# Kernel tuning notes

Measured on AMD Instinct MI355X. Metric: run time of the kernel, lower is better.

## Reference

```python
import jax, jax.numpy as jnp
import numpy as np

N, E, B, T, H, L = 8192, 2048, 512, 128, 128, 3


def setup_inputs() -> dict:
    key = jax.random.key(0)
    ks = jax.random.split(key, 14)
    # sparse binary hyperedge incidence [E, N]
    Hbat = (jax.random.uniform(ks[0], (E, N)) < 0.01).astype(jnp.float32)
    DV2 = jax.random.uniform(ks[1], (N,)) + 0.1    # D_v^{-1/2} node scaling
    invDE = jax.random.uniform(ks[2], (E,)) + 0.1  # D_e^{-1} edge scaling
    data = jax.random.randint(ks[3], (B, T), 0, N, dtype=jnp.int32)
    lens = jax.random.randint(ks[4], (B,), 1, T + 1, dtype=jnp.int32)
    data_length = jnp.sort(lens)[::-1].at[0].set(T)  # descending, max == T (pack_padded)
    poi = jax.random.normal(ks[5], (N, H), dtype=jnp.float32)
    s = 1.0 / float(np.sqrt(H))
    hgc1_w = jax.random.uniform(ks[6], (H, H), minval=-s, maxval=s)
    hgc1_b = jax.random.uniform(ks[7], (H,), minval=-s, maxval=s)
    hgc2_w = jax.random.uniform(ks[8], (H, H), minval=-s, maxval=s)
    hgc2_b = jax.random.uniform(ks[9], (H,), minval=-s, maxval=s)
    Wih = jax.random.uniform(ks[10], (L, 3 * H, H), minval=-s, maxval=s)
    Whh = jax.random.uniform(ks[11], (L, 3 * H, H), minval=-s, maxval=s)
    bih = jax.random.uniform(ks[12], (L, 3 * H), minval=-s, maxval=s)
    bhh = jax.random.uniform(ks[13], (L, 3 * H), minval=-s, maxval=s)
    return dict(Hbat=Hbat, DV2=DV2, invDE=invDE, data=data, data_length=data_length,
                poi=poi, hgc1_w=hgc1_w, hgc1_b=hgc1_b, hgc2_w=hgc2_w, hgc2_b=hgc2_b,
                Wih=Wih, Whh=Whh, bih=bih, bhh=bhh)


def _gru(x, Wih, Whh, bih, bhh):
    # torch nn.GRU (batch_first, 1 layer, h0=0). x: [B,T,H] -> [B,T,H]
    gx = jnp.einsum('bth,gh->btg', x, Wih) + bih  # precompute input gates [B,T,3H]

    def step(h, gxt):
        gh = h @ Whh.T + bhh
        xr, xz, xn = jnp.split(gxt, 3, axis=-1)
        hr, hz, hn = jnp.split(gh, 3, axis=-1)
        r = jax.nn.sigmoid(xr + hr)
        z = jax.nn.sigmoid(xz + hz)
        n = jnp.tanh(xn + r * hn)
        h_new = (1.0 - z) * n + z * h
        return h_new, h_new

    h0 = jnp.zeros((x.shape[0], x.shape[2]), x.dtype)
    _, ys = jax.lax.scan(step, h0, jnp.swapaxes(gx, 0, 1))
    return jnp.swapaxes(ys, 0, 1)


def reference(Hbat, DV2, invDE, data, data_length, poi,
              hgc1_w, hgc1_b, hgc2_w, hgc2_b, Wih, Whh, bih, bhh):
    # G = diag(DV2) Hbat^T diag(invDE) Hbat diag(DV2); diag_embed GEMMs == row/col scaling
    G = (DV2[:, None] * Hbat.T) @ (invDE[:, None] * Hbat * DV2[None, :])  # [N,N]
    x = jax.nn.relu(G @ (poi @ hgc1_w + hgc1_b)) + poi
    x = G @ (x @ hgc2_w + hgc2_b)
    batch_emb = x[data]  # [B,T,H]
    Tn = batch_emb.shape[1]
    # pad_packed_sequence zero-fills beyond each sequence's length
    mask = (jnp.arange(Tn)[None, :] < data_length[:, None])[:, :, None].astype(batch_emb.dtype)
    inp = batch_emb
    n_layers = Wih.shape[0]
    for l in range(n_layers - 1):
        out = _gru(inp, Wih[l], Whh[l], bih[l], bhh[l]) * mask
        inp = batch_emb + jax.nn.relu(out)
    out = _gru(inp, Wih[-1], Whh[-1], bih[-1], bhh[-1]) * mask
    last = out[jnp.arange(out.shape[0]), data_length - 1]  # gather last valid step
    return jnp.tanh(last)
```

## Files before the change

kernel.cpp:

```cpp
#include <hip/hip_runtime.h>

#define NN 8192
#define EE 2048
#define BB 512
#define TT 128
#define HH 128
#define G3 384
#define MAXNNZ 256
#define MAXDEG 96

typedef __attribute__((ext_vector_type(8))) _Float16 f16x8;
typedef __attribute__((ext_vector_type(4))) float f32x4;

__device__ __forceinline__ float sigm(float x){ return 1.0f/(1.0f+__expf(-x)); }
__device__ __forceinline__ float tanhfast(float x){ return 2.0f/(1.0f+__expf(-2.0f*x)) - 1.0f; }

__device__ __forceinline__ void bar_lds(){
  __builtin_amdgcn_sched_barrier(0);
  asm volatile("s_waitcnt lgkmcnt(0)\n\ts_barrier" ::: "memory");
  __builtin_amdgcn_sched_barrier(0);
}

__global__ __launch_bounds__(256)
void build_nnz(const float* __restrict__ Hb, int* __restrict__ idx, int* __restrict__ cnt){
  __shared__ int c;
  const int e = blockIdx.x;
  if (threadIdx.x == 0) c = 0;
  __syncthreads();
  const float* row = Hb + (size_t)e * NN;
  for (int n = threadIdx.x; n < NN; n += 256){
    if (row[n] != 0.0f){
      int p = atomicAdd(&c, 1);
      if (p < MAXNNZ) idx[e*MAXNNZ + p] = n;
    }
  }
  __syncthreads();
  if (threadIdx.x == 0) cnt[e] = (c < MAXNNZ ? c : MAXNNZ);
}

__global__ __launch_bounds__(128)
void build_nodelists(const int* __restrict__ idx, const int* __restrict__ cnt,
                     int* __restrict__ ndeg, int* __restrict__ nidx){
  const int e = blockIdx.x;
  const int c = cnt[e];
  for (int k = threadIdx.x; k < c; k += 128){
    int n = idx[e*MAXNNZ + k];
    int p = atomicAdd(&ndeg[n], 1);
    if (p < MAXDEG) nidx[n*MAXDEG + p] = e;
  }
}

__global__ __launch_bounds__(256)
void prep_w(const float* __restrict__ W, _Float16* __restrict__ whi,
            _Float16* __restrict__ wlo, int n){
  int i = blockIdx.x*256 + threadIdx.x;
  if (i >= n) return;
  float g = W[i] * 16.0f;
  _Float16 h = (_Float16)g;
  whi[i] = h;
  wlo[i] = (_Float16)(g - (float)h);
}

__global__ __launch_bounds__(256)
void prep_wt(const float* __restrict__ W, _Float16* __restrict__ wt_hi,
             _Float16* __restrict__ wt_lo){
  int i = blockIdx.x*256 + threadIdx.x;
  int k = i >> 7, j = i & 127;
  float g = W[i] * 16.0f;
  _Float16 h = (_Float16)g;
  wt_hi[j*HH + k] = h;
  wt_lo[j*HH + k] = (_Float16)(g - (float)h);
}

template<bool SCALE>
__global__ __launch_bounds__(256)
void mm128_mfma(const float* __restrict__ A, const _Float16* __restrict__ Bh,
                const _Float16* __restrict__ Bl, const float* __restrict__ bias,
                const float* __restrict__ rowscale, float* __restrict__ C)
{
  const int tid = threadIdx.x;
  const int w = tid >> 6, l = tid & 63;
  const int lm = l & 15, q = l >> 4;
  const int r0 = blockIdx.x * 32;
  const int n0 = w * 32;

  f32x4 acc[2][2];
  #pragma unroll
  for (int m=0;m<2;m++)
    #pragma unroll
    for (int n=0;n<2;n++) acc[m][n] = (f32x4){0.f,0.f,0.f,0.f};

  #pragma unroll 1
  for (int ks = 0; ks < 4; ++ks){
    const int kb = ks*32 + q*8;
    f16x8 ah[2], al[2];
    #pragma unroll
    for (int m=0;m<2;m++){
      const float* pa = A + (size_t)(r0 + m*16 + lm)*HH + kb;
      float4 f0 = *(const float4*)pa;
      float4 f1 = *(const float4*)(pa+4);
      float fv[8] = {f0.x,f0.y,f0.z,f0.w,f1.x,f1.y,f1.z,f1.w};
      union { f16x8 v; _Float16 u[8]; } uh, ul;
      #pragma unroll
      for (int j=0;j<8;j++){
        _Float16 hh = (_Float16)fv[j];
        uh.u[j] = hh;
        ul.u[j] = (_Float16)(fv[j] - (float)hh);
      }
      ah[m] = uh.v; al[m] = ul.v;
    }
    #pragma unroll
    for (int n=0;n<2;n++){
      const int j = n0 + n*16 + lm;
      f16x8 bh = *(const f16x8*)(Bh + (size_t)j*HH + kb);
      f16x8 bl = *(const f16x8*)(Bl + (size_t)j*HH + kb);
      #pragma unroll
      for (int m=0;m<2;m++){
        acc[m][n] = __builtin_amdgcn_mfma_f32_16x16x32_f16(ah[m], bh, acc[m][n], 0,0,0);
        acc[m][n] = __builtin_amdgcn_mfma_f32_16x16x32_f16(al[m], bh, acc[m][n], 0,0,0);
        acc[m][n] = __builtin_amdgcn_mfma_f32_16x16x32_f16(ah[m], bl, acc[m][n], 0,0,0);
      }
    }
  }
  #pragma unroll
  for (int n=0;n<2;n++){
    const int j = n0 + n*16 + lm;
    const float bv = bias[j];
    #pragma unroll
    for (int m=0;m<2;m++){
      #pragma unroll
      for (int i=0;i<4;i++){
        int r = r0 + m*16 + q*4 + i;
        float cv = acc[m][n][i]*(1.0f/16.0f) + bv;
        if (SCALE) cv *= rowscale[r];
        C[(size_t)r*HH + j] = cv;
      }
    }
  }
}

__global__ __launch_bounds__(128)
void edge_gather(const float* __restrict__ Xs, const int* __restrict__ idx,
                 const int* __restrict__ cnt, const float* __restrict__ invDE,
                 float* __restrict__ Eb){
  __shared__ int sidx[MAXNNZ];
  const int e = blockIdx.x, h = threadIdx.x;
  const int c = cnt[e];
  for (int k = h; k < c; k += 128) sidx[k] = idx[e*MAXNNZ + k];
  __syncthreads();
  float acc = 0.0f;
  int k = 0;
  for (; k + 4 <= c; k += 4){
    float a0 = Xs[(size_t)sidx[k+0]*HH + h];
    float a1 = Xs[(size_t)sidx[k+1]*HH + h];
    float a2 = Xs[(size_t)sidx[k+2]*HH + h];
    float a3 = Xs[(size_t)sidx[k+3]*HH + h];
    acc += (a0 + a1) + (a2 + a3);
  }
  for (; k < c; ++k) acc += Xs[(size_t)sidx[k]*HH + h];
  Eb[e*HH + h] = invDE[e] * acc;
}

template<int MODE>
__global__ __launch_bounds__(128)
void node_gather(const float* __restrict__ Eb, const int* __restrict__ nidx,
                 const int* __restrict__ ndeg, const float* __restrict__ DV2,
                 const float* __restrict__ poi, float* __restrict__ Xo){
  __shared__ int sidx[MAXDEG];
  const int n = blockIdx.x, h = threadIdx.x;
  int c = ndeg[n]; c = c < MAXDEG ? c : MAXDEG;
  for (int k = h; k < c; k += 128) sidx[k] = nidx[n*MAXDEG + k];
  __syncthreads();
  float acc = 0.0f;
  int k = 0;
  for (; k + 4 <= c; k += 4){
    float a0 = Eb[(size_t)sidx[k+0]*HH + h];
    float a1 = Eb[(size_t)sidx[k+1]*HH + h];
    float a2 = Eb[(size_t)sidx[k+2]*HH + h];
    float a3 = Eb[(size_t)sidx[k+3]*HH + h];
    acc += (a0 + a1) + (a2 + a3);
  }
  for (; k < c; ++k) acc += Eb[(size_t)sidx[k]*HH + h];
  float v = DV2[n] * acc;
  if (MODE == 1) Xo[(size_t)n*HH + h] = fmaxf(v, 0.0f) + poi[(size_t)n*HH + h];
  else           Xo[(size_t)n*HH + h] = v;
}

__global__ __launch_bounds__(256)
void gather_emb(const float* __restrict__ X, const int* __restrict__ data, float* __restrict__ emb){
  int r = blockIdx.x*2 + (threadIdx.x >> 7);
  int h = threadIdx.x & 127;
  int n = data[r];
  emb[(size_t)r*HH + h] = X[(size_t)n*HH + h];
}

template<bool FUSE>
__global__ __launch_bounds__(256)
void gx_gemm(const float* __restrict__ emb, const _Float16* __restrict__ hin,
             const _Float16* __restrict__ Whi, const _Float16* __restrict__ Wlo,
             const float* __restrict__ bih, const int* __restrict__ lens,
             float* __restrict__ gx)
{
  const int blk = blockIdx.x;
  const int b = blk >> 2, tt = blk & 3;
  const int lenb = lens[b];
  if (tt*32 >= lenb) return;
  const int tid = threadIdx.x;
  const int w = tid >> 6, l = tid & 63;
  const int lm = l & 15, q = l >> 4;
  const int r0 = b*TT + tt*32;
  const int n0 = w*96;

  f32x4 acc[2][6];
  #pragma unroll
  for (int m=0;m<2;m++)
    #pragma unroll
    for (int n=0;n<6;n++) acc[m][n] = (f32x4){0.f,0.f,0.f,0.f};

  #pragma unroll 1
  for (int ks = 0; ks < 4; ++ks){
    const int kb = ks*32 + q*8;
    f16x8 ah[2], al[2];
    #pragma unroll
    for (int m=0;m<2;m++){
      const size_t ro = (size_t)(r0 + m*16 + lm)*HH + kb;
      float4 f0 = *(const float4*)(emb + ro);
      float4 f1 = *(const float4*)(emb + ro + 4);
      float fv[8] = {f0.x,f0.y,f0.z,f0.w,f1.x,f1.y,f1.z,f1.w};
      if (FUSE){
        f16x8 hv = *(const f16x8*)(hin + ro);
        #pragma unroll
        for (int j=0;j<8;j++) fv[j] += fmaxf((float)hv[j], 0.0f);
      }
      union { f16x8 v; _Float16 u[8]; } uh, ul;
      #pragma unroll
      for (int j=0;j<8;j++){
        _Float16 hh = (_Float16)fv[j];
        uh.u[j] = hh;
        ul.u[j] = (_Float16)(fv[j] - (float)hh);
      }
      ah[m] = uh.v; al[m] = ul.v;
    }
    #pragma unroll
    for (int n=0;n<6;n++){
      const int g = n0 + n*16 + lm;
      f16x8 bh = *(const f16x8*)(Whi + (size_t)g*HH + kb);
      f16x8 bl = *(const f16x8*)(Wlo + (size_t)g*HH + kb);
      #pragma unroll
      for (int m=0;m<2;m++){
        acc[m][n] = __builtin_amdgcn_mfma_f32_16x16x32_f16(ah[m], bh, acc[m][n], 0,0,0);
        acc[m][n] = __builtin_amdgcn_mfma_f32_16x16x32_f16(al[m], bh, acc[m][n], 0,0,0);
        acc[m][n] = __builtin_amdgcn_mfma_f32_16x16x32_f16(ah[m], bl, acc[m][n], 0,0,0);
      }
    }
  }
  #pragma unroll
  for (int n=0;n<6;n++){
    const int g = n0 + n*16 + lm;
    const float bv = bih[g];
    #pragma unroll
    for (int m=0;m<2;m++){
      #pragma unroll
      for (int i=0;i<4;i++){
        int t = tt*32 + m*16 + q*4 + i;
        if (t < lenb)
          gx[((size_t)b*TT + t)*G3 + g] = acc[m][n][i]*(1.0f/16.0f) + bv;
      }
    }
  }
}

template<bool FINAL>
__global__ __launch_bounds__(512, 1)
void gru_scan3(const float* __restrict__ gxp, const float* __restrict__ Whh,
               const float* __restrict__ bhh, const int* __restrict__ lens,
               _Float16* __restrict__ hout, float* __restrict__ final_out)
{
  __shared__ _Float16 hbuf[2][16*HH];
  __shared__ float ghT[2][392];
  const int tid = threadIdx.x;
  const int w = tid >> 6, lane = tid & 63;
  const int lm = lane & 15, q = lane >> 4;
  const int b0 = blockIdx.x * 2;

  f16x8 wf[3][4];
  #pragma unroll
  for (int n=0; n<3; ++n){
    const int col = w*48 + n*16 + lm;
    const float* wr = Whh + (size_t)col*HH;
    #pragma unroll
    for (int ks=0; ks<4; ++ks){
      const int kb = ks*32 + q*8;
      float4 f0 = *(const float4*)(wr + kb);
      float4 f1 = *(const float4*)(wr + kb + 4);
      float fv[8] = {f0.x,f0.y,f0.z,f0.w,f1.x,f1.y,f1.z,f1.w};
      union { f16x8 v; _Float16 u[8]; } uu;
      #pragma unroll
      for (int j=0;j<8;j++) uu.u[j] = (_Float16)(fv[j] * 16.0f);
      wf[n][ks] = uu.v;
    }
  }
  const float S = 1.0f/16.0f;
  const int lenmax = lens[b0];

  const int gb = tid >> 7, gd = tid & 127;
  float bR=0.f, bZ=0.f, bN=0.f; int glen=0;
  const float* gxrow = nullptr; _Float16* hrow = nullptr;
  if (tid < 256){
    bR = bhh[gd]; bZ = bhh[HH+gd]; bN = bhh[2*HH+gd];
    glen = lens[b0+gb];
    gxrow = gxp + (size_t)(b0+gb)*TT*G3;
    if (!FINAL) hrow = hout + (size_t)(b0+gb)*TT*HH + gd;
  }

  {
    unsigned int* z = (unsigned int*)&hbuf[0][0];
    #pragma unroll 1
    for (int i = tid; i < 2*16*HH/2; i += 512) z[i] = 0u;
  }
  __syncthreads();

  float xv0=0.f, xv1=0.f, xv2=0.f, hp=0.f;
  if (tid < 256){ xv0 = gxrow[gd]; xv1 = gxrow[128+gd]; xv2 = gxrow[256+gd]; }

  int cur = 0;
  #pragma unroll 1
  for (int t = 0; t < lenmax; ++t){
    f16x8 av[4];
    #pragma unroll
    for (int ks=0; ks<4; ++ks){
      int off = (lm*256 + ks*64 + q*16) ^ ((lm & 7) << 4);
      av[ks] = *(const f16x8*)((const char*)&hbuf[cur][0] + off);
    }
    float xn0=0.f, xn1=0.f, xn2=0.f;
    if (tid < 256){
      int tp = (t+1 < lenmax) ? t+1 : t;
      const float* bgx = gxrow + (size_t)tp*G3;
      xn0 = bgx[gd]; xn1 = bgx[128+gd]; xn2 = bgx[256+gd];
    }
    f32x4 a0 = (f32x4){0.f,0.f,0.f,0.f}, a1 = a0, a2 = a0;
    #pragma unroll
    for (int ks=0; ks<4; ++ks){
      a0 = __builtin_amdgcn_mfma_f32_16x16x32_f16(av[ks], wf[0][ks], a0, 0,0,0);
      a1 = __builtin_amdgcn_mfma_f32_16x16x32_f16(av[ks], wf[1][ks], a1, 0,0,0);
      a2 = __builtin_amdgcn_mfma_f32_16x16x32_f16(av[ks], wf[2][ks], a2, 0,0,0);
    }
    if (q == 0){
      const int c0 = w*48 + lm;
      ghT[0][c0]      = a0[0];  ghT[1][c0]      = a0[1];
      ghT[0][c0+16]   = a1[0];  ghT[1][c0+16]   = a1[1];
      ghT[0][c0+32]   = a2[0];  ghT[1][c0+32]   = a2[1];
    }
    bar_lds();

    if (tid < 256){
      float gr = ghT[gb][gd], gz = ghT[gb][128+gd], gn = ghT[gb][256+gd];
      float r = sigm(xv0 + gr*S + bR);
      float z = sigm(xv1 + gz*S + bZ);
      float n = tanhfast(xv2 + r*(gn*S + bN));
      float hnew = (1.0f - z)*n + z*hp;
      hp = hnew;
      int off = (gb*256 + gd*2) ^ (gb << 4);
      *(_Float16*)((char*)&hbuf[cur^1][0] + off) = (_Float16)hnew;
      if (!FINAL){
        hrow[(size_t)t*HH] = (_Float16)hnew;
      } else {
        if (t == glen - 1)
          final_out[(size_t)(b0+gb)*HH + gd] = tanhfast(hnew);
      }
    }
    xv0 = xn0; xv1 = xn1; xv2 = xn2;
    bar_lds();
    cur ^= 1;
  }
}

extern "C" void kernel_launch(void* const* d_in, const int* in_sizes, int n_in,
                              void* d_out, int out_size, void* d_ws, size_t ws_size,
                              hipStream_t stream)
{
  const float* Hb    = (const float*)d_in[0];
  const float* DV2   = (const float*)d_in[1];
  const float* invDE = (const float*)d_in[2];
  const int*   data  = (const int*)d_in[3];
  const int*   dlen  = (const int*)d_in[4];
  const float* poi   = (const float*)d_in[5];
  const float* w1    = (const float*)d_in[6];
  const float* b1    = (const float*)d_in[7];
  const float* w2    = (const float*)d_in[8];
  const float* b2    = (const float*)d_in[9];
  const float* Wih   = (const float*)d_in[10];
  const float* Whh   = (const float*)d_in[11];
  const float* bih   = (const float*)d_in[12];
  const float* bhh   = (const float*)d_in[13];
  float* out = (float*)d_out;

  float* ws   = (float*)d_ws;
  float* x1s  = ws;
  float* x2   = x1s + (size_t)NN*HH;
  float* x3s  = x2  + (size_t)NN*HH;
  float* x4   = x3s + (size_t)NN*HH;
  float* ebuf = x4  + (size_t)NN*HH;
  int*   idx  = (int*)(ebuf + (size_t)EE*HH);
  int*   cnt  = idx + (size_t)EE*MAXNNZ;
  float* gx   = (float*)(cnt + EE);
  float* emb  = gx  + (size_t)BB*TT*G3;
  _Float16* hout = (_Float16*)(emb + (size_t)BB*TT*HH);
  _Float16* Whi  = hout + (size_t)BB*TT*HH;
  _Float16* Wlo  = Whi + (size_t)3*G3*HH;
  _Float16* w1th = Wlo + (size_t)3*G3*HH;
  _Float16* w1tl = w1th + (size_t)HH*HH;
  _Float16* w2th = w1tl + (size_t)HH*HH;
  _Float16* w2tl = w2th + (size_t)HH*HH;
  int* ndeg = (int*)(w2tl + (size_t)HH*HH);
  int* nidx = ndeg + NN;

  hipMemsetAsync(ndeg, 0, NN*sizeof(int), stream);
  build_nnz<<<EE, 256, 0, stream>>>(Hb, idx, cnt);
  build_nodelists<<<EE, 128, 0, stream>>>(idx, cnt, ndeg, nidx);
  prep_w<<<(3*G3*HH + 255)/256, 256, 0, stream>>>(Wih, Whi, Wlo, 3*G3*HH);
  prep_wt<<<HH*HH/256, 256, 0, stream>>>(w1, w1th, w1tl);
  prep_wt<<<HH*HH/256, 256, 0, stream>>>(w2, w2th, w2tl);

  mm128_mfma<true><<<NN/32, 256, 0, stream>>>(poi, w1th, w1tl, b1, DV2, x1s);
  edge_gather<<<EE, 128, 0, stream>>>(x1s, idx, cnt, invDE, ebuf);
  node_gather<1><<<NN, 128, 0, stream>>>(ebuf, nidx, ndeg, DV2, poi, x2);
  mm128_mfma<true><<<NN/32, 256, 0, stream>>>(x2, w2th, w2tl, b2, DV2, x3s);
  edge_gather<<<EE, 128, 0, stream>>>(x3s, idx, cnt, invDE, ebuf);
  node_gather<2><<<NN, 128, 0, stream>>>(ebuf, nidx, ndeg, DV2, (const float*)nullptr, x4);
  gather_emb<<<BB*TT/2, 256, 0, stream>>>(x4, data, emb);

  for (int l = 0; l < 3; ++l){
    if (l == 0)
      gx_gemm<false><<<BB*4, 256, 0, stream>>>(emb, (const _Float16*)nullptr,
          Whi + (size_t)l*G3*HH, Wlo + (size_t)l*G3*HH, bih + (size_t)l*G3, dlen, gx);
    else
      gx_gemm<true><<<BB*4, 256, 0, stream>>>(emb, hout,
          Whi + (size_t)l*G3*HH, Wlo + (size_t)l*G3*HH, bih + (size_t)l*G3, dlen, gx);
    if (l < 2)
      gru_scan3<false><<<BB/2, 512, 0, stream>>>(gx, Whh + (size_t)l*G3*HH,
          bhh + (size_t)l*G3, dlen, hout, (float*)nullptr);
    else
      gru_scan3<true><<<BB/2, 512, 0, stream>>>(gx, Whh + (size_t)l*G3*HH,
          bhh + (size_t)l*G3, dlen, (_Float16*)nullptr, out);
  }
}
```

Measured before the change: 581.5 us.

## Precompute fp16 hi/lo operand splits in producer kernels instead of in GEMMs

```diff
diff --git a/kernel.cpp b/kernel.cpp
--- a/kernel.cpp
+++ b/kernel.cpp
@@ -62,6 +62,17 @@
 }
 
 __global__ __launch_bounds__(256)
+void prep_split(const float* __restrict__ X, _Float16* __restrict__ hi,
+                _Float16* __restrict__ lo, int n){
+  int i = blockIdx.x*256 + threadIdx.x;
+  if (i >= n) return;
+  float v = X[i];
+  _Float16 h = (_Float16)v;
+  hi[i] = h;
+  lo[i] = (_Float16)(v - (float)h);
+}
+
+__global__ __launch_bounds__(256)
 void prep_wt(const float* __restrict__ W, _Float16* __restrict__ wt_hi,
              _Float16* __restrict__ wt_lo){
   int i = blockIdx.x*256 + threadIdx.x;
@@ -74,9 +85,10 @@
 
 template<bool SCALE>
 __global__ __launch_bounds__(256)
-void mm128_mfma(const float* __restrict__ A, const _Float16* __restrict__ Bh,
-                const _Float16* __restrict__ Bl, const float* __restrict__ bias,
-                const float* __restrict__ rowscale, float* __restrict__ C)
+void mm128_mfma(const _Float16* __restrict__ Ahi, const _Float16* __restrict__ Alo,
+                const _Float16* __restrict__ Bh, const _Float16* __restrict__ Bl,
+                const float* __restrict__ bias, const float* __restrict__ rowscale,
+                float* __restrict__ C)
 {
   const int tid = threadIdx.x;
   const int w = tid >> 6, l = tid & 63;
@@ -90,24 +102,15 @@
     #pragma unroll
     for (int n=0;n<2;n++) acc[m][n] = (f32x4){0.f,0.f,0.f,0.f};
 
-  #pragma unroll 1
+  #pragma unroll 2
   for (int ks = 0; ks < 4; ++ks){
     const int kb = ks*32 + q*8;
     f16x8 ah[2], al[2];
     #pragma unroll
     for (int m=0;m<2;m++){
-      const float* pa = A + (size_t)(r0 + m*16 + lm)*HH + kb;
-      float4 f0 = *(const float4*)pa;
-      float4 f1 = *(const float4*)(pa+4);
-      float fv[8] = {f0.x,f0.y,f0.z,f0.w,f1.x,f1.y,f1.z,f1.w};
-      union { f16x8 v; _Float16 u[8]; } uh, ul;
-      #pragma unroll
-      for (int j=0;j<8;j++){
-        _Float16 hh = (_Float16)fv[j];
-        uh.u[j] = hh;
-        ul.u[j] = (_Float16)(fv[j] - (float)hh);
-      }
-      ah[m] = uh.v; al[m] = ul.v;
+      const size_t ro = (size_t)(r0 + m*16 + lm)*HH + kb;
+      ah[m] = *(const f16x8*)(Ahi + ro);
+      al[m] = *(const f16x8*)(Alo + ro);
     }
     #pragma unroll
     for (int n=0;n<2;n++){
@@ -165,7 +168,8 @@
 __global__ __launch_bounds__(128)
 void node_gather(const float* __restrict__ Eb, const int* __restrict__ nidx,
                  const int* __restrict__ ndeg, const float* __restrict__ DV2,
-                 const float* __restrict__ poi, float* __restrict__ Xo){
+                 const float* __restrict__ poi, _Float16* __restrict__ ohi,
+                 _Float16* __restrict__ olo, float* __restrict__ Xo){
   __shared__ int sidx[MAXDEG];
   const int n = blockIdx.x, h = threadIdx.x;
   int c = ndeg[n]; c = c < MAXDEG ? c : MAXDEG;
@@ -182,21 +186,33 @@
   }
   for (; k < c; ++k) acc += Eb[(size_t)sidx[k]*HH + h];
   float v = DV2[n] * acc;
-  if (MODE == 1) Xo[(size_t)n*HH + h] = fmaxf(v, 0.0f) + poi[(size_t)n*HH + h];
-  else           Xo[(size_t)n*HH + h] = v;
-}
-
-__global__ __launch_bounds__(256)
-void gather_emb(const float* __restrict__ X, const int* __restrict__ data, float* __restrict__ emb){
+  if (MODE == 1){
+    float val = fmaxf(v, 0.0f) + poi[(size_t)n*HH + h];
+    _Float16 hh = (_Float16)val;
+    ohi[(size_t)n*HH + h] = hh;
+    olo[(size_t)n*HH + h] = (_Float16)(val - (float)hh);
+  } else {
+    Xo[(size_t)n*HH + h] = v;
+  }
+}
+
+__global__ __launch_bounds__(256)
+void gather_emb(const float* __restrict__ X, const int* __restrict__ data,
+                float* __restrict__ emb, _Float16* __restrict__ aHi,
+                _Float16* __restrict__ aLo){
   int r = blockIdx.x*2 + (threadIdx.x >> 7);
   int h = threadIdx.x & 127;
   int n = data[r];
-  emb[(size_t)r*HH + h] = X[(size_t)n*HH + h];
-}
-
-template<bool FUSE>
-__global__ __launch_bounds__(256)
-void gx_gemm(const float* __restrict__ emb, const _Float16* __restrict__ hin,
+  float v = X[(size_t)n*HH + h];
+  size_t o = (size_t)r*HH + h;
+  emb[o] = v;
+  _Float16 hh = (_Float16)v;
+  aHi[o] = hh;
+  aLo[o] = (_Float16)(v - (float)hh);
+}
+
+__global__ __launch_bounds__(256)
+void gx_gemm(const _Float16* __restrict__ Ahi, const _Float16* __restrict__ Alo,
              const _Float16* __restrict__ Whi, const _Float16* __restrict__ Wlo,
              const float* __restrict__ bih, const int* __restrict__ lens,
              float* __restrict__ gx)
@@ -217,29 +233,15 @@
     #pragma unroll
     for (int n=0;n<6;n++) acc[m][n] = (f32x4){0.f,0.f,0.f,0.f};
 
-  #pragma unroll 1
+  #pragma unroll 2
   for (int ks = 0; ks < 4; ++ks){
     const int kb = ks*32 + q*8;
     f16x8 ah[2], al[2];
     #pragma unroll
     for (int m=0;m<2;m++){
       const size_t ro = (size_t)(r0 + m*16 + lm)*HH + kb;
-      float4 f0 = *(const float4*)(emb + ro);
-      float4 f1 = *(const float4*)(emb + ro + 4);
-      float fv[8] = {f0.x,f0.y,f0.z,f0.w,f1.x,f1.y,f1.z,f1.w};
-      if (FUSE){
-        f16x8 hv = *(const f16x8*)(hin + ro);
-        #pragma unroll
-        for (int j=0;j<8;j++) fv[j] += fmaxf((float)hv[j], 0.0f);
-      }
-      union { f16x8 v; _Float16 u[8]; } uh, ul;
-      #pragma unroll
-      for (int j=0;j<8;j++){
-        _Float16 hh = (_Float16)fv[j];
-        uh.u[j] = hh;
-        ul.u[j] = (_Float16)(fv[j] - (float)hh);
-      }
-      ah[m] = uh.v; al[m] = ul.v;
+      ah[m] = *(const f16x8*)(Ahi + ro);
+      al[m] = *(const f16x8*)(Alo + ro);
     }
     #pragma unroll
     for (int n=0;n<6;n++){
@@ -263,8 +265,7 @@
       #pragma unroll
       for (int i=0;i<4;i++){
         int t = tt*32 + m*16 + q*4 + i;
-        if (t < lenb)
-          gx[((size_t)b*TT + t)*G3 + g] = acc[m][n][i]*(1.0f/16.0f) + bv;
+        gx[((size_t)b*TT + t)*G3 + g] = acc[m][n][i]*(1.0f/16.0f) + bv;
       }
     }
   }
@@ -274,7 +275,8 @@
 __global__ __launch_bounds__(512, 1)
 void gru_scan3(const float* __restrict__ gxp, const float* __restrict__ Whh,
                const float* __restrict__ bhh, const int* __restrict__ lens,
-               _Float16* __restrict__ hout, float* __restrict__ final_out)
+               const float* __restrict__ emb, _Float16* __restrict__ aHi,
+               _Float16* __restrict__ aLo, float* __restrict__ final_out)
 {
   __shared__ _Float16 hbuf[2][16*HH];
   __shared__ float ghT[2][392];
@@ -305,12 +307,18 @@
 
   const int gb = tid >> 7, gd = tid & 127;
   float bR=0.f, bZ=0.f, bN=0.f; int glen=0;
-  const float* gxrow = nullptr; _Float16* hrow = nullptr;
+  const float* gxrow = nullptr;
+  const float* erow = nullptr;
+  _Float16 *ahrow = nullptr, *alrow = nullptr;
   if (tid < 256){
     bR = bhh[gd]; bZ = bhh[HH+gd]; bN = bhh[2*HH+gd];
     glen = lens[b0+gb];
     gxrow = gxp + (size_t)(b0+gb)*TT*G3;
-    if (!FINAL) hrow = hout + (size_t)(b0+gb)*TT*HH + gd;
+    if (!FINAL){
+      erow  = emb + (size_t)(b0+gb)*TT*HH + gd;
+      ahrow = aHi + (size_t)(b0+gb)*TT*HH + gd;
+      alrow = aLo + (size_t)(b0+gb)*TT*HH + gd;
+    }
   }
 
   {
@@ -320,8 +328,11 @@
   }
   __syncthreads();
 
-  float xv0=0.f, xv1=0.f, xv2=0.f, hp=0.f;
-  if (tid < 256){ xv0 = gxrow[gd]; xv1 = gxrow[128+gd]; xv2 = gxrow[256+gd]; }
+  float xv0=0.f, xv1=0.f, xv2=0.f, xe=0.f, hp=0.f;
+  if (tid < 256){
+    xv0 = gxrow[gd]; xv1 = gxrow[128+gd]; xv2 = gxrow[256+gd];
+    if (!FINAL) xe = erow[0];
+  }
 
   int cur = 0;
   #pragma unroll 1
@@ -332,11 +343,12 @@
       int off = (lm*256 + ks*64 + q*16) ^ ((lm & 7) << 4);
       av[ks] = *(const f16x8*)((const char*)&hbuf[cur][0] + off);
     }
-    float xn0=0.f, xn1=0.f, xn2=0.f;
+    float xn0=0.f, xn1=0.f, xn2=0.f, xen=0.f;
     if (tid < 256){
       int tp = (t+1 < lenmax) ? t+1 : t;
       const float* bgx = gxrow + (size_t)tp*G3;
       xn0 = bgx[gd]; xn1 = bgx[128+gd]; xn2 = bgx[256+gd];
+      if (!FINAL) xen = erow[(size_t)tp*HH];
     }
     f32x4 a0 = (f32x4){0.f,0.f,0.f,0.f}, a1 = a0, a2 = a0;
     #pragma unroll
@@ -363,13 +375,16 @@
       int off = (gb*256 + gd*2) ^ (gb << 4);
       *(_Float16*)((char*)&hbuf[cur^1][0] + off) = (_Float16)hnew;
       if (!FINAL){
-        hrow[(size_t)t*HH] = (_Float16)hnew;
+        float a = xe + fmaxf(hnew, 0.0f);
+        _Float16 ah = (_Float16)a;
+        ahrow[(size_t)t*HH] = ah;
+        alrow[(size_t)t*HH] = (_Float16)(a - (float)ah);
       } else {
         if (t == glen - 1)
           final_out[(size_t)(b0+gb)*HH + gd] = tanhfast(hnew);
       }
     }
-    xv0 = xn0; xv1 = xn1; xv2 = xn2;
+    xv0 = xn0; xv1 = xn1; xv2 = xn2; xe = xen;
     bar_lds();
     cur ^= 1;
   }
@@ -397,22 +412,26 @@
 
   float* ws   = (float*)d_ws;
   float* x1s  = ws;
-  float* x2   = x1s + (size_t)NN*HH;
-  float* x3s  = x2  + (size_t)NN*HH;
+  float* x3s  = x1s + (size_t)NN*HH;
   float* x4   = x3s + (size_t)NN*HH;
   float* ebuf = x4  + (size_t)NN*HH;
-  int*   idx  = (int*)(ebuf + (size_t)EE*HH);
-  int*   cnt  = idx + (size_t)EE*MAXNNZ;
-  float* gx   = (float*)(cnt + EE);
+  float* gx   = ebuf + (size_t)EE*HH;
   float* emb  = gx  + (size_t)BB*TT*G3;
-  _Float16* hout = (_Float16*)(emb + (size_t)BB*TT*HH);
-  _Float16* Whi  = hout + (size_t)BB*TT*HH;
+  _Float16* aHi  = (_Float16*)(emb + (size_t)BB*TT*HH);
+  _Float16* aLo  = aHi + (size_t)BB*TT*HH;
+  _Float16* x2hi = aLo + (size_t)BB*TT*HH;
+  _Float16* x2lo = x2hi + (size_t)NN*HH;
+  _Float16* pHi  = x2lo + (size_t)NN*HH;
+  _Float16* pLo  = pHi + (size_t)NN*HH;
+  _Float16* Whi  = pLo + (size_t)NN*HH;
   _Float16* Wlo  = Whi + (size_t)3*G3*HH;
   _Float16* w1th = Wlo + (size_t)3*G3*HH;
   _Float16* w1tl = w1th + (size_t)HH*HH;
   _Float16* w2th = w1tl + (size_t)HH*HH;
   _Float16* w2tl = w2th + (size_t)HH*HH;
-  int* ndeg = (int*)(w2tl + (size_t)HH*HH);
+  int* idx  = (int*)(w2tl + (size_t)HH*HH);
+  int* cnt  = idx + (size_t)EE*MAXNNZ;
+  int* ndeg = cnt + EE;
   int* nidx = ndeg + NN;
 
   hipMemsetAsync(ndeg, 0, NN*sizeof(int), stream);
@@ -421,27 +440,26 @@
   prep_w<<<(3*G3*HH + 255)/256, 256, 0, stream>>>(Wih, Whi, Wlo, 3*G3*HH);
   prep_wt<<<HH*HH/256, 256, 0, stream>>>(w1, w1th, w1tl);
   prep_wt<<<HH*HH/256, 256, 0, stream>>>(w2, w2th, w2tl);
-
-  mm128_mfma<true><<<NN/32, 256, 0, stream>>>(poi, w1th, w1tl, b1, DV2, x1s);
+  prep_split<<<NN*HH/256, 256, 0, stream>>>(poi, pHi, pLo, NN*HH);
+
+  mm128_mfma<true><<<NN/32, 256, 0, stream>>>(pHi, pLo, w1th, w1tl, b1, DV2, x1s);
   edge_gather<<<EE, 128, 0, stream>>>(x1s, idx, cnt, invDE, ebuf);
-  node_gather<1><<<NN, 128, 0, stream>>>(ebuf, nidx, ndeg, DV2, poi, x2);
-  mm128_mfma<true><<<NN/32, 256, 0, stream>>>(x2, w2th, w2tl, b2, DV2, x3s);
+  node_gather<1><<<NN, 128, 0, stream>>>(ebuf, nidx, ndeg, DV2, poi, x2hi, x2lo, (float*)nullptr);
+  mm128_mfma<true><<<NN/32, 256, 0, stream>>>(x2hi, x2lo, w2th, w2tl, b2, DV2, x3s);
   edge_gather<<<EE, 128, 0, stream>>>(x3s, idx, cnt, invDE, ebuf);
-  node_gather<2><<<NN, 128, 0, stream>>>(ebuf, nidx, ndeg, DV2, (const float*)nullptr, x4);
-  gather_emb<<<BB*TT/2, 256, 0, stream>>>(x4, data, emb);
+  node_gather<2><<<NN, 128, 0, stream>>>(ebuf, nidx, ndeg, DV2, (const float*)nullptr,
+                                         (_Float16*)nullptr, (_Float16*)nullptr, x4);
+  gather_emb<<<BB*TT/2, 256, 0, stream>>>(x4, data, emb, aHi, aLo);
 
   for (int l = 0; l < 3; ++l){
-    if (l == 0)
-      gx_gemm<false><<<BB*4, 256, 0, stream>>>(emb, (const _Float16*)nullptr,
-          Whi + (size_t)l*G3*HH, Wlo + (size_t)l*G3*HH, bih + (size_t)l*G3, dlen, gx);
-    else
-      gx_gemm<true><<<BB*4, 256, 0, stream>>>(emb, hout,
-          Whi + (size_t)l*G3*HH, Wlo + (size_t)l*G3*HH, bih + (size_t)l*G3, dlen, gx);
+    gx_gemm<<<BB*4, 256, 0, stream>>>(aHi, aLo, Whi + (size_t)l*G3*HH,
+        Wlo + (size_t)l*G3*HH, bih + (size_t)l*G3, dlen, gx);
     if (l < 2)
       gru_scan3<false><<<BB/2, 512, 0, stream>>>(gx, Whh + (size_t)l*G3*HH,
-          bhh + (size_t)l*G3, dlen, hout, (float*)nullptr);
+          bhh + (size_t)l*G3, dlen, emb, aHi, aLo, (float*)nullptr);
     else
       gru_scan3<true><<<BB/2, 512, 0, stream>>>(gx, Whh + (size_t)l*G3*HH,
-          bhh + (size_t)l*G3, dlen, (_Float16*)nullptr, out);
-  }
-}
+          bhh + (size_t)l*G3, dlen, (const float*)nullptr,
+          (_Float16*)nullptr, (_Float16*)nullptr, out);
+  }
+}
```

New measurement: 580.4 us. About the same (-0.2%).
